# Kernel optimization log

Measured on AMD Instinct MI355X. Metric: run time of the kernel, lower is better.

Reference implementation:

```python
import jax, jax.numpy as jnp
import numpy as np

PAD, BOS = 0, 1
EPS = 1e-08


def _lstm_cell(xt, h, c, wih, whh, bih, bhh):
    z = xt @ wih.T + h @ whh.T + bih + bhh
    i, f, g, o = jnp.split(z, 4, axis=-1)  # torch gate order i,f,g,o
    c = jax.nn.sigmoid(f) * c + jax.nn.sigmoid(i) * jnp.tanh(g)
    h = jax.nn.sigmoid(o) * jnp.tanh(c)
    return h, c


def _run_lstm(emb, wih, whh, bih, bhh):
    B, H = emb.shape[0], whh.shape[1]
    def step(carry, xt):
        h, c = _lstm_cell(xt, carry[0], carry[1], wih, whh, bih, bhh)
        return (h, c), h
    init = (jnp.zeros((B, H), emb.dtype), jnp.zeros((B, H), emb.dtype))
    (hT, cT), outs = jax.lax.scan(step, init, jnp.swapaxes(emb, 0, 1))
    return jnp.swapaxes(outs, 0, 1), hT, cT


def setup_inputs() -> dict:
    key = jax.random.key(0)
    V, H, B, S, T = 32000, 256, 8, 200, 51
    ks = jax.random.split(key, 24)
    def n(i, shape, s=0.02):
        return jax.random.normal(ks[i], shape, jnp.float32) * s
    x = jax.random.randint(ks[0], (B, S), 1, V)
    x = x.at[:, -1].set(V - 1)  # pins extended vocab size to 2V
    labels = jax.random.randint(ks[1], (B, T), 1, V)
    return {
        "x": x, "labels": labels, "ext_vocab_size": 2 * V,
        "emb_enc": n(2, (V, H)).at[PAD].set(0.0),
        "wih_f": n(3, (4 * H, H)), "whh_f": n(4, (4 * H, H)),
        "bih_f": jnp.zeros((4 * H,), jnp.float32), "bhh_f": jnp.zeros((4 * H,), jnp.float32),
        "wih_b": n(5, (4 * H, H)), "whh_b": n(6, (4 * H, H)),
        "bih_b": jnp.zeros((4 * H,), jnp.float32), "bhh_b": jnp.zeros((4 * H,), jnp.float32),
        "w_sel1": n(7, (H, 2 * H)), "b_sel1": jnp.zeros((H,), jnp.float32),
        "w_sel2": n(8, (1, H)), "b_sel2": jnp.zeros((1,), jnp.float32),
        "w_rh": n(9, (H, 2 * H)), "b_rh": jnp.zeros((H,), jnp.float32),
        "w_rc": n(10, (H, 2 * H)), "b_rc": jnp.zeros((H,), jnp.float32),
        "emb_dec": n(11, (V, H)).at[PAD].set(0.0),
        "wih_d": n(12, (4 * H, 3 * H)), "whh_d": n(13, (4 * H, H)),
        "bih_d": jnp.zeros((4 * H,), jnp.float32), "bhh_d": jnp.zeros((4 * H,), jnp.float32),
        "w_attn": n(14, (H, 4 * H)), "b_attn": jnp.zeros((H,), jnp.float32),
        "w_attn_v": n(15, (1, H)),
        "w_ptr": n(16, (1, 3 * H)), "b_ptr": jnp.zeros((1,), jnp.float32),
        "w_gen": n(17, (V, H)), "b_gen": jnp.zeros((V,), jnp.float32),
        "w_cov": n(18, (H, 1)), "b_cov": jnp.zeros((H,), jnp.float32),
    }


def reference(x, labels, ext_vocab_size, emb_enc, wih_f, whh_f, bih_f, bhh_f,
              wih_b, whh_b, bih_b, bhh_b, w_sel1, b_sel1, w_sel2, b_sel2,
              w_rh, b_rh, w_rc, b_rc, emb_dec, wih_d, whh_d, bih_d, bhh_d,
              w_attn, b_attn, w_attn_v, w_ptr, b_ptr, w_gen, b_gen, w_cov, b_cov):
    B, S = x.shape
    V, H = w_gen.shape
    # ---- Encoder: BiLSTM (no padding -> packing is identity; eval -> no dropout)
    emb = emb_enc[x]  # [B,S,H]
    out_f, h_f, c_f = _run_lstm(emb, wih_f, whh_f, bih_f, bhh_f)
    out_b_r, h_b, c_b = _run_lstm(emb[:, ::-1], wih_b, whh_b, bih_b, bhh_b)
    enc_out = jnp.concatenate([out_f, out_b_r[:, ::-1]], axis=-1)  # [B,S,2H]
    copy_probs = jax.nn.sigmoid(
        (jnp.tanh(enc_out @ w_sel1.T + b_sel1) @ w_sel2.T + b_sel2)[..., 0])  # [B,S]
    # ---- bidirectional state reduction
    h0 = jax.nn.relu(jnp.concatenate([h_f, h_b], -1) @ w_rh.T + b_rh)
    c0 = jax.nn.relu(jnp.concatenate([c_f, c_b], -1) @ w_rc.T + b_rc)
    # ---- Decoder loop (teacher forcing): inputs = [BOS, labels[:,1:T-1]]
    dec_in = jnp.concatenate(
        [jnp.full((B, 1), BOS, labels.dtype), labels[:, 1:-1]], axis=1)  # [B,T-1]
    mask_cp = (copy_probs > EPS).astype(jnp.float32)
    rows = jnp.arange(B)[:, None]

    def step(carry, tok):
        h, c, cov = carry
        cov_feat = cov[..., None] * w_cov[:, 0] + b_cov  # [B,S,H]
        feats = jnp.concatenate(
            [enc_out, jnp.broadcast_to(h[:, None, :], (B, S, H)), cov_feat], axis=-1)
        e = jnp.tanh(feats @ w_attn.T + b_attn)           # [B,S,H]
        attn = jax.nn.softmax(e @ w_attn_v[0], axis=1)    # [B,S]
        attn = attn * mask_cp
        attn = attn / (attn.sum(1, keepdims=True) + 1e-10)
        cov = cov + attn
        ctx = jnp.einsum('bs,bsd->bd', attn, enc_out)     # [B,2H]
        h, c = _lstm_cell(jnp.concatenate([emb_dec[tok], ctx], -1), h, c,
                          wih_d, whh_d, bih_d, bhh_d)
        p_gen = jax.nn.sigmoid(jnp.concatenate([ctx, h], -1) @ w_ptr.T + b_ptr)  # [B,1]
        vocab_dist = jax.nn.softmax(h @ w_gen.T + b_gen, axis=-1)  # [B,V]
        dist = jnp.zeros((B, ext_vocab_size), jnp.float32)
        dist = dist.at[:, :V].set(p_gen * vocab_dist)
        dist = dist.at[rows, x].add((1.0 - p_gen) * attn)  # pointer/copy scatter-add
        return (h, c, cov), dist

    cov0 = jnp.zeros((B, S), jnp.float32)
    _, outs = jax.lax.scan(step, (h0, c0, cov0), dec_in.T)
    outputs = jnp.swapaxes(outs, 0, 1)  # [B,T-1,EV]
    # ---- loss (faithful: CE treats the mixture distribution as logits)
    targets = labels[:, 1:]
    logp = jax.nn.log_softmax(outputs, axis=-1)
    nll = -jnp.take_along_axis(logp, targets[..., None], axis=-1)[..., 0]
    valid = (targets != PAD).astype(jnp.float32)
    loss_ce = (nll * valid).sum() / valid.sum()
    m = (x != PAD).astype(jnp.float32)
    lp = jnp.clip(jnp.log(copy_probs), -100.0, None)
    l1p = jnp.clip(jnp.log1p(-copy_probs), -100.0, None)
    bce = -(m * lp + (1.0 - m) * l1p)
    loss = loss_ce + 1.0 * (bce * m).sum() / m.sum()
    return outputs, loss
```

## Files before the change

### kernel.cpp

```cpp
#include <hip/hip_runtime.h>
#include <hip/hip_bf16.h>
#include <stdint.h>


#define DEVI __device__ __forceinline__
#define AT_RLX __ATOMIC_RELAXED
#define SC_AGT __HIP_MEMORY_SCOPE_AGENT

static constexpr size_t OFF_ACC   = 0;
static constexpr size_t OFF_FLAGE = 4;
static constexpr size_t OFF_FLAGD = 36;
static constexpr size_t ZERO_FLOATS = 200;
static constexpr size_t OFF_CTX   = 256;
static constexpr size_t OFF_EMB   = 4352;
static constexpr size_t OFF_HSEL  = OFF_EMB;
static constexpr size_t OFF_HP    = OFF_EMB;
static constexpr size_t OFF_DHP   = OFF_EMB;
static constexpr size_t OFF_DCX   = OFF_EMB + 8192;
static constexpr size_t DTAG_FLOATS = 16384;
static constexpr size_t OFF_PREF  = OFF_EMB  + 409600;
static constexpr size_t OFF_PREB  = OFF_PREF + 1638400;
static constexpr size_t OFF_BIAS  = OFF_PREB + 1638400;
static constexpr size_t OFF_HB    = OFF_BIAS + 3072;
static constexpr size_t OFF_HFIN  = OFF_HB   + 8192;
static constexpr size_t OFF_CFIN  = OFF_HFIN + 4096;
static constexpr size_t OFF_ENCOUT= OFF_CFIN + 4096;
static constexpr size_t OFF_MASK  = OFF_ENCOUT + 819200;
static constexpr size_t OFF_C0    = OFF_MASK + 1600;
static constexpr size_t OFF_EP    = OFF_C0   + 2048;
static constexpr size_t OFF_WCP   = OFF_EP   + 409600;
static constexpr size_t OFF_BCP   = OFF_WCP  + 256;
static constexpr size_t OFF_DEMB  = OFF_BCP  + 256;
static constexpr size_t OFF_DPRE  = OFF_DEMB + 102400;
static constexpr size_t OFF_HBUF  = OFF_DPRE + 409600;
static constexpr size_t OFF_CS    = OFF_HBUF + 4096;
static constexpr size_t OFF_HS    = OFF_CS   + 204800;
static constexpr size_t OFF_AS    = OFF_HS   + 102400;
static constexpr size_t OFF_PG    = OFF_AS   + 80000;
static constexpr size_t OFF_PE    = OFF_PG   + 512;

DEVI float sigf(float x)      { return 1.0f / (1.0f + __expf(-x)); }
DEVI float tanh_fast(float x) { return 1.0f - 2.0f / (1.0f + __expf(2.0f * x)); }
DEVI float ald(const float* p)  { return __hip_atomic_load((float*)p, AT_RLX, SC_AGT); }
DEVI void  ast(float* p, float v){ __hip_atomic_store(p, v, AT_RLX, SC_AGT); }
DEVI unsigned long long aldu(const unsigned long long* p) {
  return __hip_atomic_load((unsigned long long*)p, AT_RLX, SC_AGT);
}
DEVI void astu(unsigned long long* p, unsigned long long v) {
  __hip_atomic_store(p, v, AT_RLX, SC_AGT);
}

__global__ __launch_bounds__(256) void k_biassum(
    const float* bih_f, const float* bhh_f, const float* bih_b, const float* bhh_b,
    const float* bih_d, const float* bhh_d, float* ws) {
  int i = blockIdx.x * 256 + threadIdx.x;
  int which = i >> 10, jj = i & 1023;
  float v = (which == 0) ? bih_f[jj] + bhh_f[jj]
          : (which == 1) ? bih_b[jj] + bhh_b[jj]
                         : bih_d[jj] + bhh_d[jj];
  ws[OFF_BIAS + i] = v;
}

__global__ __launch_bounds__(256) void k_embed(
    const int* xin, const int* labels, const float* emb_enc, const float* emb_dec, float* ws) {
  int r = blockIdx.x, h = threadIdx.x;
  if (r < 1600) {
    int t = r >> 3, b = r & 7;
    ws[OFF_EMB + (size_t)r * 256 + h] = emb_enc[(size_t)xin[b * 200 + t] * 256 + h];
  } else {
    int r2 = r - 1600;
    int t = r2 >> 3, b = r2 & 7;
    int tok = (t == 0) ? 1 : labels[b * 51 + t];
    ws[OFF_DEMB + (size_t)r2 * 256 + h] = emb_dec[(size_t)tok * 256 + h];
  }
}

template<int BM, int BN, int TM, int TN, int CMAP, int ACT, int AMAP>
__global__ __launch_bounds__(256) void k_gemm(
    const float* __restrict__ A, const float* __restrict__ B,
    const float* __restrict__ bias, float* __restrict__ C,
    int M, int K, int ldb, int ldc) {
  __shared__ float As[16][BM];
  __shared__ float Bs[16][BN];
  const int tid = threadIdx.x;
  const int tx = tid & 15, ty = tid >> 4;
  const int m0 = blockIdx.x * BM, n0 = blockIdx.y * BN;
  float acc[TM][TN];
#pragma unroll
  for (int i = 0; i < TM; ++i)
#pragma unroll
    for (int q = 0; q < TN; ++q) acc[i][q] = 0.f;

  for (int kk = 0; kk < K; kk += 16) {
#pragma unroll
    for (int e = tid; e < BM * 4; e += 256) {
      int m = e >> 2, k4 = (e & 3) * 4;
      int gm0 = m0 + m;
      float4 v = {0.f, 0.f, 0.f, 0.f};
      if (gm0 < M) {
        int gm = AMAP ? (((199 - (gm0 >> 3)) << 3) + (gm0 & 7)) : gm0;
        v = *(const float4*)(A + (size_t)gm * K + kk + k4);
      }
      As[k4 + 0][m] = v.x; As[k4 + 1][m] = v.y; As[k4 + 2][m] = v.z; As[k4 + 3][m] = v.w;
    }
#pragma unroll
    for (int e = tid; e < BN * 4; e += 256) {
      int n = e >> 2, k4 = (e & 3) * 4;
      float4 v = *(const float4*)(B + (size_t)(n0 + n) * ldb + kk + k4);
      Bs[k4 + 0][n] = v.x; Bs[k4 + 1][n] = v.y; Bs[k4 + 2][n] = v.z; Bs[k4 + 3][n] = v.w;
    }
    __syncthreads();
#pragma unroll
    for (int k = 0; k < 16; ++k) {
      float a[TM], bv[TN];
#pragma unroll
      for (int i = 0; i < TM; ++i) a[i] = As[k][ty * TM + i];
#pragma unroll
      for (int q = 0; q < TN; ++q) bv[q] = Bs[k][tx * TN + q];
#pragma unroll
      for (int i = 0; i < TM; ++i)
#pragma unroll
        for (int q = 0; q < TN; ++q) acc[i][q] += a[i] * bv[q];
    }
    __syncthreads();
  }
#pragma unroll
  for (int i = 0; i < TM; ++i) {
    int gm = m0 + ty * TM + i;
    if (gm >= M) continue;
    size_t base;
    if (CMAP == 1) { int t = gm >> 3, b = gm & 7; base = (size_t)(b * 50 + t) * 64000; }
    else            base = (size_t)gm * ldc;
#pragma unroll
    for (int q = 0; q < TN; ++q) {
      int n = n0 + tx * TN + q;
      float v = acc[i][q] + bias[n];
      if (ACT == 1) v = tanh_fast(v);
      C[base + n] = v;
    }
  }
}

__global__ __launch_bounds__(512, 1) void k_encoder(
    const float* __restrict__ whh_f, const float* __restrict__ whh_b, float* __restrict__ ws) {
  __shared__ float hs2[2048];
  __shared__ float zs[512];
  const int dir = blockIdx.x >> 4;
  const int p   = blockIdx.x & 15;
  const int u0  = p * 16;
  const float* whh = dir ? whh_b : whh_f;
  const float* pre = ws + (dir ? OFF_PREB : OFF_PREF);
  unsigned long long* hp = (unsigned long long*)(ws + OFF_HP);
  const int tid = threadIdx.x;
  const int kc4 = tid & 15;
  const int jp  = tid >> 4;
  const int jj0 = jp * 2, jj1 = jj0 + 1;
  const int jg0 = (jj0 >> 4) * 256 + u0 + (jj0 & 15);
  const int jg1 = (jj1 >> 4) * 256 + u0 + (jj1 & 15);
  float4 W0[4], W1[4];
  {
    const float* w0 = whh + (size_t)jg0 * 256 + kc4 * 16;
    const float* w1 = whh + (size_t)jg1 * 256 + kc4 * 16;
#pragma unroll
    for (int q = 0; q < 4; ++q) { W0[q] = *(const float4*)(w0 + q * 4);
                                  W1[q] = *(const float4*)(w1 + q * 4); }
  }
  const int jlf = kc4 >> 3, bf = kc4 & 7;
  const int jjf = jp * 2 + jlf;
  const int jf  = (jjf >> 4) * 256 + u0 + (jjf & 15);
  const int zsl = (jjf >> 4) * 128 + (jjf & 15) * 8 + bf;
  const int wb_ = tid >> 6;
  const int kk0 = (tid * 4) & 255;
  const int wdst = wb_ * 256 + ((kk0 >> 2) & 3) * 64 + (kk0 >> 4) * 4;
  const int ui2 = tid & 15, b2 = tid >> 4;
  float c_reg = 0.f;
  float* enc = ws + OFF_ENCOUT;

  for (int t = 0; t < 200; ++t) {
    float pre_v = pre[((size_t)t * 8 + bf) * 1024 + jf];
    float acc[16];
#pragma unroll
    for (int i = 0; i < 16; ++i) acc[i] = 0.f;
    if (t > 0) {
      unsigned long long* src = hp + (size_t)((((t + 1) & 1) * 2 + dir) * 2048) + tid * 4;
      const unsigned long long e = (unsigned long long)(unsigned)t;
      unsigned long long a0, a1, a2, a3;
      for (;;) {
        a0 = aldu(src + 0); a1 = aldu(src + 1); a2 = aldu(src + 2); a3 = aldu(src + 3);
        if (((a0 >> 32) == e) && ((a1 >> 32) == e) &&
            ((a2 >> 32) == e) && ((a3 >> 32) == e)) break;
        __builtin_amdgcn_s_sleep(1);
      }
      float4 hv;
      hv.x = __uint_as_float((unsigned)a0);
      hv.y = __uint_as_float((unsigned)a1);
      hv.z = __uint_as_float((unsigned)a2);
      hv.w = __uint_as_float((unsigned)a3);
      *(float4*)(&hs2[wdst]) = hv;
    }
    __syncthreads();
    if (t > 0) {
#pragma unroll
      for (int b = 0; b < 8; ++b) {
        const float* hb = &hs2[b * 256 + kc4 * 4];
#pragma unroll
        for (int q = 0; q < 4; ++q) {
          float4 h4 = *(const float4*)(hb + q * 64);
          acc[b]     = fmaf(W0[q].x, h4.x, acc[b]);
          acc[b]     = fmaf(W0[q].y, h4.y, acc[b]);
          acc[b]     = fmaf(W0[q].z, h4.z, acc[b]);
          acc[b]     = fmaf(W0[q].w, h4.w, acc[b]);
          acc[8 + b] = fmaf(W1[q].x, h4.x, acc[8 + b]);
          acc[8 + b] = fmaf(W1[q].y, h4.y, acc[8 + b]);
          acc[8 + b] = fmaf(W1[q].z, h4.z, acc[8 + b]);
          acc[8 + b] = fmaf(W1[q].w, h4.w, acc[8 + b]);
        }
      }
    }
    {
      bool h8 = (kc4 & 8) != 0;
#pragma unroll
      for (int i = 0; i < 8; ++i) {
        float send = h8 ? acc[i] : acc[i + 8];
        float keep = h8 ? acc[i + 8] : acc[i];
        acc[i] = keep + __shfl_xor(send, 8);
      }
      bool h4b = (kc4 & 4) != 0;
#pragma unroll
      for (int i = 0; i < 4; ++i) {
        float send = h4b ? acc[i] : acc[i + 4];
        float keep = h4b ? acc[i + 4] : acc[i];
        acc[i] = keep + __shfl_xor(send, 4);
      }
      bool h2b = (kc4 & 2) != 0;
#pragma unroll
      for (int i = 0; i < 2; ++i) {
        float send = h2b ? acc[i] : acc[i + 2];
        float keep = h2b ? acc[i + 2] : acc[i];
        acc[i] = keep + __shfl_xor(send, 2);
      }
      bool h1b = (kc4 & 1) != 0;
      {
        float send = h1b ? acc[0] : acc[1];
        float keep = h1b ? acc[1] : acc[0];
        acc[0] = keep + __shfl_xor(send, 1);
      }
    }
    zs[zsl] = acc[0] + pre_v;
    __syncthreads();
    if (tid < 128) {
      int i0 = ui2 * 8 + b2;
      float zi = zs[i0], zf = zs[128 + i0], zg = zs[256 + i0], zo = zs[384 + i0];
      float cn = sigf(zf) * c_reg + sigf(zi) * tanh_fast(zg);
      float hn = sigf(zo) * tanh_fast(cn);
      c_reg = cn;
      int uu = u0 + ui2;
      if (t < 199) {
        unsigned long long pk =
            ((unsigned long long)(unsigned)(t + 1) << 32) |
            (unsigned long long)__float_as_uint(hn);
        astu(hp + (size_t)(((t & 1) * 2 + dir) * 2048) + b2 * 256 + uu, pk);
      }
      int s = dir ? (199 - t) : t;
      enc[((size_t)b2 * 200 + s) * 512 + dir * 256 + uu] = hn;
      if (t == 199) {
        ws[OFF_HFIN + (size_t)(dir * 8 + b2) * 256 + uu] = hn;
        ws[OFF_CFIN + (size_t)(dir * 8 + b2) * 256 + uu] = cn;
      }
    }
  }
}

__global__ __launch_bounds__(64) void k_selbce(
    const float* w_sel2, const float* b_sel2, const int* xin, float* ws) {
  int r = blockIdx.x, lane = threadIdx.x;
  float pacc = 0.f;
#pragma unroll
  for (int i = 0; i < 4; ++i) {
    int k = lane + 64 * i;
    pacc += ws[OFF_HSEL + (size_t)r * 256 + k] * w_sel2[k];
  }
#pragma unroll
  for (int m = 1; m < 64; m <<= 1) pacc += __shfl_xor(pacc, m);
  if (lane == 0) {
    float cp = sigf(pacc + b_sel2[0]);
    ws[OFF_MASK + r] = (cp > 1e-8f) ? 1.f : 0.f;
    int b = r / 200, s = r % 200;
    float m = (xin[b * 200 + s] != 0) ? 1.f : 0.f;
    if (m > 0.f) {
      float lp = fmaxf(logf(cp), -100.f);
      atomicAdd(ws + OFF_ACC + 2, -lp);
    }
    atomicAdd(ws + OFF_ACC + 3, m);
  }
}

__global__ __launch_bounds__(256) void k_wcp(
    const float* w_attn, const float* w_cov, const float* b_cov, float* ws) {
  int jj = threadIdx.x;
  float a = 0.f, c = 0.f;
  for (int h = 0; h < 256; ++h) {
    float w = w_attn[(size_t)jj * 1024 + 768 + h];
    a += w * w_cov[h];
    c += w * b_cov[h];
  }
  ws[OFF_WCP + jj] = a;
  ws[OFF_BCP + jj] = c;
}

__global__ __launch_bounds__(256) void k_h0c0(
    const float* w_rh, const float* b_rh, const float* w_rc, const float* b_rc, float* ws) {
  int b = blockIdx.x, jj = threadIdx.x;
  const float* hf  = ws + OFF_HFIN + (size_t)b * 256;
  const float* hbk = ws + OFF_HFIN + 2048 + (size_t)b * 256;
  const float* cf  = ws + OFF_CFIN + (size_t)b * 256;
  const float* cbk = ws + OFF_CFIN + 2048 + (size_t)b * 256;
  float ah = b_rh[jj], ac = b_rc[jj];
  for (int k = 0; k < 256; ++k) {
    ah += hf[k] * w_rh[(size_t)jj * 512 + k];
    ac += cf[k] * w_rc[(size_t)jj * 512 + k];
  }
  for (int k = 0; k < 256; ++k) {
    ah += hbk[k] * w_rh[(size_t)jj * 512 + 256 + k];
    ac += cbk[k] * w_rc[(size_t)jj * 512 + 256 + k];
  }
  ws[OFF_C0 + (size_t)b * 256 + jj] = fmaxf(ac, 0.f);
  unsigned long long* hp2 = (unsigned long long*)(ws + OFF_DHP);
  hp2[(size_t)b * 256 + jj] = (unsigned long long)__float_as_uint(fmaxf(ah, 0.f));
}

__global__ __launch_bounds__(512, 1) void k_decoder(
    const float* __restrict__ wih_d, const float* __restrict__ whh_d,
    const float* __restrict__ w_attn, const float* __restrict__ w_attn_v,
    float* __restrict__ ws) {
  __shared__ float hc_s[8 * 768];
  __shared__ float h_pad[264];
  __shared__ float hw_s[256];
  __shared__ float e_s[200];
  __shared__ float at_s[200], cv_s[200], msk_s[200];
  __shared__ float zs_l[256];
  __shared__ float wc_s[256], bc_s[256], wv_s[256];
  __shared__ float mS_s[2];
  __shared__ float cxp_s[4][128];
  const int g = blockIdx.x, tid = threadIdx.x;
  const int b1 = g >> 2, sq = g & 3, s0 = sq * 50;
  unsigned long long* hp2 = (unsigned long long*)(ws + OFF_DHP);
  unsigned long long* cx2 = (unsigned long long*)(ws + OFF_DCX);
  const int jW = tid >> 1, khW = tid & 1;
  float4 W32[32];
#pragma unroll
  for (int q = 0; q < 32; ++q)
    W32[q] = *(const float4*)(w_attn + (size_t)jW * 1024 + 512 + khW * 128 + q * 4);
  const int kseg = tid & 15, row_l = tid >> 4;
  const int u_l = row_l & 7, gate = row_l >> 3;
  const int j = gate * 256 + g * 8 + u_l;
  float4 W48[12];
#pragma unroll
  for (int q = 0; q < 12; ++q) {
    int k0 = 4 * kseg + 64 * q;
    W48[q] = (k0 < 512) ? *(const float4*)(wih_d + (size_t)j * 768 + 256 + k0)
                        : *(const float4*)(whh_d + (size_t)j * 256 + (k0 - 512));
  }
  const int sE = tid >> 1, hE = tid & 1;
  const int cC = tid & 127, qC = tid >> 7;
  const int u_c = tid & 7, b_c = tid >> 3;
  float c_reg = (tid < 64) ? ws[OFF_C0 + (size_t)b_c * 256 + g * 8 + u_c] : 0.f;
  if (tid < 200) {
    msk_s[tid] = ws[OFF_MASK + b1 * 200 + tid];
    cv_s[tid] = 0.f;
  }
  if (tid < 256) {
    wc_s[tid] = ws[OFF_WCP + tid];
    bc_s[tid] = ws[OFF_BCP + tid];
    wv_s[tid] = w_attn_v[tid];
  }
  __syncthreads();

  for (int t = 0; t < 50; ++t) {
    const int rb = t & 1, wb = 1 - rb;
    const unsigned long long tgH = (unsigned long long)(unsigned)t;
    const unsigned long long tgP = (unsigned long long)(unsigned)(t + 1);
    if (tid < 256) {
      unsigned long long* src = hp2 + (size_t)rb * 2048 + b1 * 256 + tid;
      unsigned long long v;
      for (;;) {
        v = aldu(src);
        if ((v >> 32) == tgH) break;
        __builtin_amdgcn_s_sleep(1);
      }
      h_pad[(tid >> 5) * 33 + (tid & 31)] = __uint_as_float((unsigned)v);
    }
    __syncthreads();
    {
      float a = 0.f;
#pragma unroll
      for (int q = 0; q < 32; ++q) {
        int k = khW * 128 + q * 4;
        const float* hq = &h_pad[(k >> 5) * 33 + (k & 31)];
        float4 w4 = W32[q];
        a = fmaf(w4.x, hq[0], a);
        a = fmaf(w4.y, hq[1], a);
        a = fmaf(w4.z, hq[2], a);
        a = fmaf(w4.w, hq[3], a);
      }
      a += __shfl_xor(a, 1);
      if (khW == 0) hw_s[jW] = a;
    }
    __syncthreads();
    if (sE < 200) {
      float cv = cv_s[sE];
      const float* ep  = ws + OFF_EP + ((size_t)(b1 * 200 + sE)) * 256 + hE * 128;
      const float* hwp = &hw_s[hE * 128];
      const float* wcp = &wc_s[hE * 128];
      const float* bcp = &bc_s[hE * 128];
      const float* wvp = &wv_s[hE * 128];
      float pe = 0.f;
#pragma unroll
      for (int i4 = 0; i4 < 32; ++i4) {
        float4 e4 = *(const float4*)(ep + i4 * 4);
        float4 h4 = *(const float4*)(hwp + i4 * 4);
        float4 w4 = *(const float4*)(wcp + i4 * 4);
        float4 b4 = *(const float4*)(bcp + i4 * 4);
        float4 v4 = *(const float4*)(wvp + i4 * 4);
        pe = fmaf(tanh_fast(e4.x + h4.x + cv * w4.x + b4.x), v4.x, pe);
        pe = fmaf(tanh_fast(e4.y + h4.y + cv * w4.y + b4.y), v4.y, pe);
        pe = fmaf(tanh_fast(e4.z + h4.z + cv * w4.z + b4.z), v4.z, pe);
        pe = fmaf(tanh_fast(e4.w + h4.w + cv * w4.w + b4.w), v4.w, pe);
      }
      pe += __shfl_xor(pe, 1);
      if (hE == 0) e_s[sE] = pe;
    }
    __syncthreads();
    if (tid < 64) {
      float m = -1e30f;
#pragma unroll
      for (int i = 0; i < 4; ++i) {
        int s = tid + 64 * i;
        if (s < 200) m = fmaxf(m, e_s[s]);
      }
#pragma unroll
      for (int md = 1; md < 64; md <<= 1) m = fmaxf(m, __shfl_xor(m, md));
      float es = 0.f, ems = 0.f;
#pragma unroll
      for (int i = 0; i < 4; ++i) {
        int s = tid + 64 * i;
        if (s < 200) {
          float e = __expf(e_s[s] - m);
          es += e; ems += e * msk_s[s];
        }
      }
#pragma unroll
      for (int md = 1; md < 64; md <<= 1) { es += __shfl_xor(es, md); ems += __shfl_xor(ems, md); }
      if (tid == 0) { mS_s[0] = m; mS_s[1] = 1.0f / (ems + 1e-10f * es); }
    }
    __syncthreads();
    if (tid < 200) {
      float a = __expf(e_s[tid] - mS_s[0]) * msk_s[tid] * mS_s[1];
      at_s[tid] = a;
      cv_s[tid] += a;
      if (tid >= s0 && tid < s0 + 50)
        ws[OFF_AS + ((size_t)t * 8 + b1) * 200 + tid] = a;
    }
    __syncthreads();
    {
      float ca = 0.f;
      const float* ebase = ws + OFF_ENCOUT + ((size_t)(b1 * 200 + qC * 50)) * 512 + sq * 128 + cC;
#pragma unroll 10
      for (int s2 = 0; s2 < 50; ++s2)
        ca = fmaf(at_s[qC * 50 + s2], ebase[(size_t)s2 * 512], ca);
      cxp_s[qC][cC] = ca;
    }
    __syncthreads();
    if (tid < 128) {
      float ca = (cxp_s[0][tid] + cxp_s[1][tid]) + (cxp_s[2][tid] + cxp_s[3][tid]);
      astu(cx2 + (size_t)b1 * 512 + sq * 128 + tid,
           (tgP << 32) | (unsigned long long)__float_as_uint(ca));
    }
    for (int e = tid; e < 6144; e += 512) {
      int bb = e / 768, kk2 = e % 768;
      float val;
      if (kk2 < 512) {
        unsigned long long* src = cx2 + (size_t)bb * 512 + kk2;
        unsigned long long v;
        for (;;) {
          v = aldu(src);
          if ((v >> 32) == tgP) break;
          __builtin_amdgcn_s_sleep(1);
        }
        val = __uint_as_float((unsigned)v);
      } else {
        unsigned long long* src = hp2 + (size_t)rb * 2048 + bb * 256 + (kk2 - 512);
        unsigned long long v;
        for (;;) {
          v = aldu(src);
          if ((v >> 32) == tgH) break;
          __builtin_amdgcn_s_sleep(1);
        }
        val = __uint_as_float((unsigned)v);
      }
      hc_s[e] = val;
    }
    __syncthreads();
    if (g < 8) ws[OFF_CS + ((size_t)t * 8 + g) * 512 + tid] = hc_s[g * 768 + tid];
    float acc[8];
#pragma unroll
    for (int b = 0; b < 8; ++b) acc[b] = 0.f;
#pragma unroll
    for (int q = 0; q < 12; ++q) {
      int k0 = 4 * kseg + 64 * q;
#pragma unroll
      for (int b = 0; b < 8; ++b) {
        float4 h4 = *(const float4*)(&hc_s[b * 768 + k0]);
        acc[b] = fmaf(W48[q].x, h4.x, acc[b]);
        acc[b] = fmaf(W48[q].y, h4.y, acc[b]);
        acc[b] = fmaf(W48[q].z, h4.z, acc[b]);
        acc[b] = fmaf(W48[q].w, h4.w, acc[b]);
      }
    }
    {
      bool h8 = (kseg & 8) != 0;
#pragma unroll
      for (int i = 0; i < 4; ++i) {
        float send = h8 ? acc[i] : acc[i + 4];
        float keep = h8 ? acc[i + 4] : acc[i];
        acc[i] = keep + __shfl_xor(send, 8);
      }
      bool h4b = (kseg & 4) != 0;
#pragma unroll
      for (int i = 0; i < 2; ++i) {
        float send = h4b ? acc[i] : acc[i + 2];
        float keep = h4b ? acc[i + 2] : acc[i];
        acc[i] = keep + __shfl_xor(send, 4);
      }
      bool h2b = (kseg & 2) != 0;
      {
        float send = h2b ? acc[0] : acc[1];
        float keep = h2b ? acc[1] : acc[0];
        acc[0] = keep + __shfl_xor(send, 2);
      }
      acc[0] += __shfl_xor(acc[0], 1);
    }
    {
      int bz = kseg >> 1;
      float z = acc[0] + ws[OFF_DPRE + ((size_t)t * 8 + bz) * 1024 + j];
      if ((kseg & 1) == 0) zs_l[row_l * 8 + bz] = z;
    }
    __syncthreads();
    if (tid < 64) {
      float zi = zs_l[(0  + u_c) * 8 + b_c];
      float zf = zs_l[(8  + u_c) * 8 + b_c];
      float zg = zs_l[(16 + u_c) * 8 + b_c];
      float zo = zs_l[(24 + u_c) * 8 + b_c];
      float cn = sigf(zf) * c_reg + sigf(zi) * tanh_fast(zg);
      float hn = sigf(zo) * tanh_fast(cn);
      c_reg = cn;
      astu(hp2 + (size_t)wb * 2048 + b_c * 256 + g * 8 + u_c,
           (tgP << 32) | (unsigned long long)__float_as_uint(hn));
      ws[OFF_HS + ((size_t)t * 8 + b_c) * 256 + g * 8 + u_c] = hn;
    }
  }
}

__global__ __launch_bounds__(64) void k_pgen(const float* w_ptr, const float* b_ptr, float* ws) {
  int r = blockIdx.x, lane = threadIdx.x;
  float p = 0.f;
#pragma unroll
  for (int i = 0; i < 12; ++i) {
    int k = lane + 64 * i;
    float v = (k < 512) ? ws[OFF_CS + (size_t)r * 512 + k]
                        : ws[OFF_HS + (size_t)r * 256 + (k - 512)];
    p += v * w_ptr[k];
  }
#pragma unroll
  for (int m = 1; m < 64; m <<= 1) p += __shfl_xor(p, m);
  if (lane == 0) ws[OFF_PG + r] = sigf(p + b_ptr[0]);
}

__global__ __launch_bounds__(256) void k_v2(const int* xin, const int* labels, float* ws, float* out) {
  __shared__ float redm[256], reds[256];
  __shared__ int xv[200];
  __shared__ float s1sh, corrsh;
  int r = blockIdx.x, tid = threadIdx.x;
  int tt = r >> 3, b = r & 7;
  float* row = out + (size_t)(b * 50 + tt) * 64000;
  for (int i = tid; i < 200; i += 256) xv[i] = xin[b * 200 + i];
  float m = -1e30f, s = 0.f;
  for (int i = tid; i < 32000; i += 256) {
    float z = row[i];
    float nm = fmaxf(m, z);
    s = s * __expf(m - nm) + __expf(z - nm);
    m = nm;
  }
  redm[tid] = m; reds[tid] = s;
  __syncthreads();
  for (int st = 128; st >= 1; st >>= 1) {
    if (tid < st) {
      float m2 = redm[tid + st], s2 = reds[tid + st];
      float M = fmaxf(redm[tid], m2);
      reds[tid] = reds[tid] * __expf(redm[tid] - M) + s2 * __expf(m2 - M);
      redm[tid] = M;
    }
    __syncthreads();
  }
  float mx = redm[0], sum = reds[0];
  float pg = ws[OFF_PG + r];
  __syncthreads();
  float s1 = 0.f;
  float inv = 1.0f / sum;
  for (int i = tid; i < 32000; i += 256) {
    float z = row[i];
    float d = pg * (__expf(z - mx) * inv);
    row[i] = d;
    s1 += __expf(d);
  }
  for (int i = 32000 + tid; i < 64000; i += 256) row[i] = 0.0f;
  reds[tid] = s1;
  __syncthreads();
  for (int st = 128; st >= 1; st >>= 1) { if (tid < st) reds[tid] += reds[tid + st]; __syncthreads(); }
  if (tid == 0) { s1sh = reds[0]; corrsh = 0.f; }
  __syncthreads();
  if (tid < 200) {
    int v = xv[tid];
    bool own = true;
    for (int s2 = 0; s2 < tid; ++s2) if (xv[s2] == v) { own = false; break; }
    if (own) {
      float delta = 0.f;
      for (int s2 = tid; s2 < 200; ++s2)
        if (xv[s2] == v) delta += ws[OFF_AS + (size_t)r * 200 + s2];
      delta *= (1.0f - pg);
      float base = row[v];
      row[v] = base + delta;
      atomicAdd(&corrsh, __expf(base + delta) - __expf(base));
    }
  }
  __syncthreads();
  if (tid == 0) {
    float lse = logf(s1sh + corrsh + 32000.0f);
    int tgt = labels[b * 51 + tt + 1];
    float dt = row[tgt];
    float valid = (tgt != 0) ? 1.f : 0.f;
    atomicAdd(ws + OFF_ACC + 0, valid * (lse - dt));
    atomicAdd(ws + OFF_ACC + 1, valid);
  }
}

__global__ void k_loss(float* ws, float* out, int out_size) {
  out[out_size - 1] = ws[OFF_ACC + 0] / ws[OFF_ACC + 1] + ws[OFF_ACC + 2] / ws[OFF_ACC + 3];
}

extern "C" void kernel_launch(void* const* d_in, const int* in_sizes, int n_in,
                              void* d_out, int out_size, void* d_ws, size_t ws_size,
                              hipStream_t stream) {
  (void)in_sizes; (void)n_in; (void)ws_size;
  const int*   x       = (const int*)  d_in[0];
  const int*   labels  = (const int*)  d_in[1];
  const float* emb_enc = (const float*)d_in[3];
  const float* wih_f   = (const float*)d_in[4];
  const float* whh_f   = (const float*)d_in[5];
  const float* bih_f   = (const float*)d_in[6];
  const float* bhh_f   = (const float*)d_in[7];
  const float* wih_b   = (const float*)d_in[8];
  const float* whh_b   = (const float*)d_in[9];
  const float* bih_b   = (const float*)d_in[10];
  const float* bhh_b   = (const float*)d_in[11];
  const float* w_sel1  = (const float*)d_in[12];
  const float* b_sel1  = (const float*)d_in[13];
  const float* w_sel2  = (const float*)d_in[14];
  const float* b_sel2  = (const float*)d_in[15];
  const float* w_rh    = (const float*)d_in[16];
  const float* b_rh    = (const float*)d_in[17];
  const float* w_rc    = (const float*)d_in[18];
  const float* b_rc    = (const float*)d_in[19];
  const float* emb_dec = (const float*)d_in[20];
  const float* wih_d   = (const float*)d_in[21];
  const float* whh_d   = (const float*)d_in[22];
  const float* bih_d   = (const float*)d_in[23];
  const float* bhh_d   = (const float*)d_in[24];
  const float* w_attn  = (const float*)d_in[25];
  const float* b_attn  = (const float*)d_in[26];
  const float* w_attn_v= (const float*)d_in[27];
  const float* w_ptr   = (const float*)d_in[28];
  const float* b_ptr   = (const float*)d_in[29];
  const float* w_gen   = (const float*)d_in[30];
  const float* b_gen   = (const float*)d_in[31];
  const float* w_cov   = (const float*)d_in[32];
  const float* b_cov   = (const float*)d_in[33];
  float* ws  = (float*)d_ws;
  float* out = (float*)d_out;

  hipMemsetAsync(d_ws, 0, ZERO_FLOATS * 4, stream);
  k_biassum<<<12, 256, 0, stream>>>(bih_f, bhh_f, bih_b, bhh_b, bih_d, bhh_d, ws);
  k_embed<<<2000, 256, 0, stream>>>(x, labels, emb_enc, emb_dec, ws);
  k_gemm<64,64,4,4,0,0,0><<<dim3(25,16), 256, 0, stream>>>(ws+OFF_EMB,  wih_f, ws+OFF_BIAS,      ws+OFF_PREF, 1600, 256, 256, 1024);
  k_gemm<64,64,4,4,0,0,1><<<dim3(25,16), 256, 0, stream>>>(ws+OFF_EMB,  wih_b, ws+OFF_BIAS+1024, ws+OFF_PREB, 1600, 256, 256, 1024);
  k_gemm<64,64,4,4,0,0,0><<<dim3(7,16),  256, 0, stream>>>(ws+OFF_DEMB, wih_d, ws+OFF_BIAS+2048, ws+OFF_DPRE, 400,  256, 768, 1024);
  hipMemsetAsync((void*)(ws + OFF_HP), 0, (size_t)2 * 2 * 2048 * sizeof(unsigned long long), stream);
  k_encoder<<<32, 512, 0, stream>>>(whh_f, whh_b, ws);
  k_gemm<64,64,4,4,0,1,0><<<dim3(25,4),  256, 0, stream>>>(ws+OFF_ENCOUT, w_sel1, b_sel1, ws+OFF_HSEL, 1600, 512, 512, 256);
  k_selbce<<<1600, 64, 0, stream>>>(w_sel2, b_sel2, x, ws);
  hipMemsetAsync((void*)(ws + OFF_EMB), 0, DTAG_FLOATS * sizeof(float), stream);
  k_gemm<64,64,4,4,0,0,0><<<dim3(25,4),  256, 0, stream>>>(ws+OFF_ENCOUT, w_attn, b_attn, ws+OFF_EP, 1600, 512, 1024, 256);
  k_wcp<<<1, 256, 0, stream>>>(w_attn, w_cov, b_cov, ws);
  k_h0c0<<<8, 256, 0, stream>>>(w_rh, b_rh, w_rc, b_rc, ws);
  k_decoder<<<32, 512, 0, stream>>>(wih_d, whh_d, w_attn, w_attn_v, ws);
  k_pgen<<<400, 64, 0, stream>>>(w_ptr, b_ptr, ws);
  k_gemm<128,128,8,8,1,0,0><<<dim3(4,250), 256, 0, stream>>>(ws+OFF_HS, w_gen, b_gen, out, 400, 256, 256, 64000);
  k_v2<<<400, 256, 0, stream>>>(x, labels, ws, out);
  k_loss<<<1, 1, 0, stream>>>(ws, out, out_size);
}
```

Before: 2.505 ms.

## Split decoder attention energies across blocks with partial softmax stats exchange

```diff
diff --git a/kernel.cpp b/kernel.cpp
--- a/kernel.cpp
+++ b/kernel.cpp
@@ -16,8 +16,9 @@
 static constexpr size_t OFF_HSEL  = OFF_EMB;
 static constexpr size_t OFF_HP    = OFF_EMB;
 static constexpr size_t OFF_DHP   = OFF_EMB;
-static constexpr size_t OFF_DCX   = OFF_EMB + 8192;
-static constexpr size_t DTAG_FLOATS = 16384;
+static constexpr size_t OFF_DST   = OFF_EMB + 8192;
+static constexpr size_t OFF_DCX   = OFF_EMB + 8384;
+static constexpr size_t DTAG_FLOATS = 41152;
 static constexpr size_t OFF_PREF  = OFF_EMB  + 409600;
 static constexpr size_t OFF_PREB  = OFF_PREF + 1638400;
 static constexpr size_t OFF_BIAS  = OFF_PREB + 1638400;
@@ -37,7 +38,7 @@
 static constexpr size_t OFF_HS    = OFF_CS   + 204800;
 static constexpr size_t OFF_AS    = OFF_HS   + 102400;
 static constexpr size_t OFF_PG    = OFF_AS   + 80000;
-static constexpr size_t OFF_PE    = OFF_PG   + 512;
+static constexpr size_t OFF_SCL   = OFF_PG   + 512;
 
 DEVI float sigf(float x)      { return 1.0f / (1.0f + __expf(-x)); }
 DEVI float tanh_fast(float x) { return 1.0f - 2.0f / (1.0f + __expf(2.0f * x)); }
@@ -336,21 +337,27 @@
   __shared__ float hc_s[8 * 768];
   __shared__ float h_pad[264];
   __shared__ float hw_s[256];
-  __shared__ float e_s[200];
-  __shared__ float at_s[200], cv_s[200], msk_s[200];
+  __shared__ float e_loc[64];
+  __shared__ float at_s[64], cv_s[64], msk_s[64];
   __shared__ float zs_l[256];
   __shared__ float wc_s[256], bc_s[256], wv_s[256];
-  __shared__ float mS_s[2];
-  __shared__ float cxp_s[4][128];
+  __shared__ float mm_s[3];
+  __shared__ float sts_s[96];
+  __shared__ float esc_s[32], invD_s[8];
   const int g = blockIdx.x, tid = threadIdx.x;
   const int b1 = g >> 2, sq = g & 3, s0 = sq * 50;
   unsigned long long* hp2 = (unsigned long long*)(ws + OFF_DHP);
+  unsigned long long* st2 = (unsigned long long*)(ws + OFF_DST);
   unsigned long long* cx2 = (unsigned long long*)(ws + OFF_DCX);
   const int jW = tid >> 1, khW = tid & 1;
   float4 W32[32];
 #pragma unroll
   for (int q = 0; q < 32; ++q)
     W32[q] = *(const float4*)(w_attn + (size_t)jW * 1024 + 512 + khW * 128 + q * 4);
+#pragma unroll
+  for (int q = 0; q < 32; ++q)
+    asm volatile("" : "+v"(W32[q].x), "+v"(W32[q].y), "+v"(W32[q].z), "+v"(W32[q].w));
+  const int sL = tid >> 3, jh = tid & 7;
   const int kseg = tid & 15, row_l = tid >> 4;
   const int u_l = row_l & 7, gate = row_l >> 3;
   const int j = gate * 256 + g * 8 + u_l;
@@ -361,12 +368,10 @@
     W48[q] = (k0 < 512) ? *(const float4*)(wih_d + (size_t)j * 768 + 256 + k0)
                         : *(const float4*)(whh_d + (size_t)j * 256 + (k0 - 512));
   }
-  const int sE = tid >> 1, hE = tid & 1;
-  const int cC = tid & 127, qC = tid >> 7;
   const int u_c = tid & 7, b_c = tid >> 3;
   float c_reg = (tid < 64) ? ws[OFF_C0 + (size_t)b_c * 256 + g * 8 + u_c] : 0.f;
-  if (tid < 200) {
-    msk_s[tid] = ws[OFF_MASK + b1 * 200 + tid];
+  if (tid < 64) {
+    msk_s[tid] = (tid < 50) ? ws[OFF_MASK + b1 * 200 + s0 + tid] : 0.f;
     cv_s[tid] = 0.f;
   }
   if (tid < 256) {
@@ -407,87 +412,103 @@
       if (khW == 0) hw_s[jW] = a;
     }
     __syncthreads();
-    if (sE < 200) {
-      float cv = cv_s[sE];
-      const float* ep  = ws + OFF_EP + ((size_t)(b1 * 200 + sE)) * 256 + hE * 128;
-      const float* hwp = &hw_s[hE * 128];
-      const float* wcp = &wc_s[hE * 128];
-      const float* bcp = &bc_s[hE * 128];
-      const float* wvp = &wv_s[hE * 128];
+    if (sL < 50) {
+      float cv = cv_s[sL];
+      const float* ep = ws + OFF_EP + ((size_t)(b1 * 200 + s0 + sL)) * 256;
       float pe = 0.f;
 #pragma unroll
-      for (int i4 = 0; i4 < 32; ++i4) {
-        float4 e4 = *(const float4*)(ep + i4 * 4);
-        float4 h4 = *(const float4*)(hwp + i4 * 4);
-        float4 w4 = *(const float4*)(wcp + i4 * 4);
-        float4 b4 = *(const float4*)(bcp + i4 * 4);
-        float4 v4 = *(const float4*)(wvp + i4 * 4);
+      for (int q = 0; q < 8; ++q) {
+        int j4 = jh * 32 + ((q + jh) & 7) * 4;
+        float4 e4 = *(const float4*)(ep + j4);
+        float4 h4 = *(const float4*)(&hw_s[j4]);
+        float4 w4 = *(const float4*)(&wc_s[j4]);
+        float4 b4 = *(const float4*)(&bc_s[j4]);
+        float4 v4 = *(const float4*)(&wv_s[j4]);
         pe = fmaf(tanh_fast(e4.x + h4.x + cv * w4.x + b4.x), v4.x, pe);
         pe = fmaf(tanh_fast(e4.y + h4.y + cv * w4.y + b4.y), v4.y, pe);
         pe = fmaf(tanh_fast(e4.z + h4.z + cv * w4.z + b4.z), v4.z, pe);
         pe = fmaf(tanh_fast(e4.w + h4.w + cv * w4.w + b4.w), v4.w, pe);
       }
       pe += __shfl_xor(pe, 1);
-      if (hE == 0) e_s[sE] = pe;
+      pe += __shfl_xor(pe, 2);
+      pe += __shfl_xor(pe, 4);
+      if (jh == 0) e_loc[sL] = pe;
     }
     __syncthreads();
     if (tid < 64) {
-      float m = -1e30f;
-#pragma unroll
-      for (int i = 0; i < 4; ++i) {
-        int s = tid + 64 * i;
-        if (s < 200) m = fmaxf(m, e_s[s]);
-      }
+      float e = (tid < 50) ? e_loc[tid] : -1e30f;
+      float m = e;
 #pragma unroll
       for (int md = 1; md < 64; md <<= 1) m = fmaxf(m, __shfl_xor(m, md));
-      float es = 0.f, ems = 0.f;
-#pragma unroll
-      for (int i = 0; i < 4; ++i) {
-        int s = tid + 64 * i;
-        if (s < 200) {
-          float e = __expf(e_s[s] - m);
-          es += e; ems += e * msk_s[s];
-        }
-      }
+      float ex = (tid < 50) ? __expf(e - m) : 0.f;
+      float es = ex, ems = ex * msk_s[tid];
 #pragma unroll
       for (int md = 1; md < 64; md <<= 1) { es += __shfl_xor(es, md); ems += __shfl_xor(ems, md); }
-      if (tid == 0) { mS_s[0] = m; mS_s[1] = 1.0f / (ems + 1e-10f * es); }
-    }
-    __syncthreads();
-    if (tid < 200) {
-      float a = __expf(e_s[tid] - mS_s[0]) * msk_s[tid] * mS_s[1];
-      at_s[tid] = a;
-      cv_s[tid] += a;
-      if (tid >= s0 && tid < s0 + 50)
-        ws[OFF_AS + ((size_t)t * 8 + b1) * 200 + tid] = a;
+      if (tid == 0) { mm_s[0] = m; mm_s[1] = es; mm_s[2] = ems; }
+    }
+    __syncthreads();
+    if (tid < 3)
+      astu(st2 + (size_t)(b1 * 4 + sq) * 3 + tid,
+           (tgP << 32) | (unsigned long long)__float_as_uint(mm_s[tid]));
+    if (tid < 50) {
+      float ar = __expf(e_loc[tid] - mm_s[0]) * msk_s[tid];
+      at_s[tid] = ar;
+      ws[OFF_AS + ((size_t)t * 8 + b1) * 200 + s0 + tid] = ar;
     }
     __syncthreads();
     {
       float ca = 0.f;
-      const float* ebase = ws + OFF_ENCOUT + ((size_t)(b1 * 200 + qC * 50)) * 512 + sq * 128 + cC;
+      const float* ebase = ws + OFF_ENCOUT + ((size_t)(b1 * 200 + s0)) * 512 + tid;
 #pragma unroll 10
       for (int s2 = 0; s2 < 50; ++s2)
-        ca = fmaf(at_s[qC * 50 + s2], ebase[(size_t)s2 * 512], ca);
-      cxp_s[qC][cC] = ca;
-    }
-    __syncthreads();
-    if (tid < 128) {
-      float ca = (cxp_s[0][tid] + cxp_s[1][tid]) + (cxp_s[2][tid] + cxp_s[3][tid]);
-      astu(cx2 + (size_t)b1 * 512 + sq * 128 + tid,
+        ca = fmaf(at_s[s2], ebase[(size_t)s2 * 512], ca);
+      astu(cx2 + (size_t)(b1 * 4 + sq) * 512 + tid,
            (tgP << 32) | (unsigned long long)__float_as_uint(ca));
     }
+    if (tid < 96) {
+      unsigned long long* src = st2 + tid;
+      unsigned long long v;
+      for (;;) {
+        v = aldu(src);
+        if ((v >> 32) == tgP) break;
+        __builtin_amdgcn_s_sleep(1);
+      }
+      sts_s[tid] = __uint_as_float((unsigned)v);
+    }
+    __syncthreads();
+    if (tid < 8) {
+      float m0 = sts_s[tid * 12 + 0], m1 = sts_s[tid * 12 + 3],
+            m2 = sts_s[tid * 12 + 6], m3 = sts_s[tid * 12 + 9];
+      float M = fmaxf(fmaxf(m0, m1), fmaxf(m2, m3));
+      float r0 = __expf(m0 - M), r1 = __expf(m1 - M), r2 = __expf(m2 - M), r3 = __expf(m3 - M);
+      esc_s[tid * 4 + 0] = r0; esc_s[tid * 4 + 1] = r1;
+      esc_s[tid * 4 + 2] = r2; esc_s[tid * 4 + 3] = r3;
+      float ES  = r0 * sts_s[tid * 12 + 1] + r1 * sts_s[tid * 12 + 4] +
+                  r2 * sts_s[tid * 12 + 7] + r3 * sts_s[tid * 12 + 10];
+      float EMS = r0 * sts_s[tid * 12 + 2] + r1 * sts_s[tid * 12 + 5] +
+                  r2 * sts_s[tid * 12 + 8] + r3 * sts_s[tid * 12 + 11];
+      invD_s[tid] = 1.0f / (EMS + 1e-10f * ES);
+    }
+    __syncthreads();
     for (int e = tid; e < 6144; e += 512) {
       int bb = e / 768, kk2 = e % 768;
       float val;
       if (kk2 < 512) {
-        unsigned long long* src = cx2 + (size_t)bb * 512 + kk2;
-        unsigned long long v;
+        unsigned long long* p0 = cx2 + (size_t)(bb * 4 + 0) * 512 + kk2;
+        unsigned long long* p1 = cx2 + (size_t)(bb * 4 + 1) * 512 + kk2;
+        unsigned long long* p2 = cx2 + (size_t)(bb * 4 + 2) * 512 + kk2;
+        unsigned long long* p3 = cx2 + (size_t)(bb * 4 + 3) * 512 + kk2;
+        unsigned long long v0, v1, v2, v3;
         for (;;) {
-          v = aldu(src);
-          if ((v >> 32) == tgP) break;
+          v0 = aldu(p0); v1 = aldu(p1); v2 = aldu(p2); v3 = aldu(p3);
+          if (((v0 >> 32) == tgP) && ((v1 >> 32) == tgP) &&
+              ((v2 >> 32) == tgP) && ((v3 >> 32) == tgP)) break;
           __builtin_amdgcn_s_sleep(1);
         }
-        val = __uint_as_float((unsigned)v);
+        val = (esc_s[bb * 4 + 0] * __uint_as_float((unsigned)v0) +
+               esc_s[bb * 4 + 1] * __uint_as_float((unsigned)v1) +
+               esc_s[bb * 4 + 2] * __uint_as_float((unsigned)v2) +
+               esc_s[bb * 4 + 3] * __uint_as_float((unsigned)v3)) * invD_s[bb];
       } else {
         unsigned long long* src = hp2 + (size_t)rb * 2048 + bb * 256 + (kk2 - 512);
         unsigned long long v;
@@ -558,6 +579,10 @@
            (tgP << 32) | (unsigned long long)__float_as_uint(hn));
       ws[OFF_HS + ((size_t)t * 8 + b_c) * 256 + g * 8 + u_c] = hn;
     }
+    if (tid < 50)
+      cv_s[tid] += at_s[tid] * esc_s[b1 * 4 + sq] * invD_s[b1];
+    if (tid == 0)
+      ws[OFF_SCL + ((size_t)t * 8 + b1) * 4 + sq] = esc_s[b1 * 4 + sq] * invD_s[b1];
   }
 }
 
@@ -626,7 +651,8 @@
     if (own) {
       float delta = 0.f;
       for (int s2 = tid; s2 < 200; ++s2)
-        if (xv[s2] == v) delta += ws[OFF_AS + (size_t)r * 200 + s2];
+        if (xv[s2] == v)
+          delta += ws[OFF_AS + (size_t)r * 200 + s2] * ws[OFF_SCL + (size_t)r * 4 + s2 / 50];
       delta *= (1.0f - pg);
       float base = row[v];
       row[v] = base + delta;
```

Measured after the change: 2.437 ms. 2.7% less time.
